# Kernel optimization log

Hardware: AMD Instinct MI355X
Metric: run time of the kernel (lower is better)

The kernel has to match this reference:

```python
import jax, jax.numpy as jnp
import numpy as np

D_MODEL, HID, N_NODES, NODE_DIM = 128, 256, 17, 32

def _gelu(x):
    return jax.nn.gelu(x, approximate=False)  # torch nn.GELU default (erf)

def setup_inputs() -> dict:
    key = jax.random.key(0)
    ks = jax.random.split(key, 12)
    B, W = 16, 4096
    x = jax.random.normal(ks[0], (B, W, D_MODEL), dtype=jnp.float32)
    # node_proj: Linear(128,256) -> GELU -> Linear(256, 17*32)
    W1 = jax.random.normal(ks[1], (D_MODEL, HID), dtype=jnp.float32) / np.sqrt(D_MODEL)
    b1 = jnp.zeros((HID,), jnp.float32)
    W2 = jax.random.normal(ks[2], (HID, N_NODES * NODE_DIM), dtype=jnp.float32) / np.sqrt(HID)
    b2 = jnp.zeros((N_NODES * NODE_DIM,), jnp.float32)
    # GAT1
    adj1 = jnp.eye(N_NODES, dtype=jnp.float32) * 5.0 + jax.random.normal(ks[3], (N_NODES, N_NODES), jnp.float32) * 0.05
    Wg1 = jax.random.normal(ks[4], (NODE_DIM, NODE_DIM), dtype=jnp.float32) / np.sqrt(NODE_DIM)
    bg1 = jnp.zeros((NODE_DIM,), jnp.float32)
    # GAT2
    adj2 = jnp.eye(N_NODES, dtype=jnp.float32) * 5.0 + jax.random.normal(ks[5], (N_NODES, N_NODES), jnp.float32) * 0.05
    Wg2 = jax.random.normal(ks[6], (NODE_DIM, NODE_DIM), dtype=jnp.float32) / np.sqrt(NODE_DIM)
    bg2 = jnp.zeros((NODE_DIM,), jnp.float32)
    # coord_proj: Linear(32, 2)
    Wc = jax.random.normal(ks[7], (NODE_DIM, 2), dtype=jnp.float32) / np.sqrt(NODE_DIM)
    bc = jnp.zeros((2,), jnp.float32)
    return {"x": x, "W1": W1, "b1": b1, "W2": W2, "b2": b2,
            "adj1": adj1, "Wg1": Wg1, "bg1": bg1,
            "adj2": adj2, "Wg2": Wg2, "bg2": bg2,
            "Wc": Wc, "bc": bc}

def _gat(nodes, adj_logits, Wg, bg):
    # nodes: [B, W, N, F]
    adj = jax.nn.softmax(adj_logits, axis=-1)          # [N, N]
    mixed = jnp.einsum('ij,bwjf->bwif', adj, nodes)    # graph conv over 17 joints
    return _gelu(mixed @ Wg + bg) + nodes              # linear-GELU + residual

def reference(x, W1, b1, W2, b2, adj1, Wg1, bg1, adj2, Wg2, bg2, Wc, bc):
    B, W, _ = x.shape
    h = _gelu(x @ W1 + b1)                 # [B, W, 256] (dropout inactive at eval)
    nodes = (h @ W2 + b2).reshape(B, W, N_NODES, NODE_DIM)
    out = _gat(nodes, adj1, Wg1, bg1)
    out = _gat(out, adj2, Wg2, bg2)
    return out @ Wc + bc                   # [B, W, 17, 2]
```

## Files before the change

### kernel.cpp

```cpp
#include <hip/hip_runtime.h>
#include <hip/hip_bf16.h>

using bf16 = __hip_bfloat16;
typedef __bf16 bf16x8 __attribute__((ext_vector_type(8)));
typedef float f32x4 __attribute__((ext_vector_type(4)));

#define MT 32
#define SX 136
#define SH 264
#define SN 552
#define SM 40

__device__ __forceinline__ float bf2f(bf16 v) { return __bfloat162float(v); }

__device__ __forceinline__ float gelu_f(float x) {
    float u  = 0.7978845608f * x * (1.0f + 0.044715f * x * x);
    float au = fabsf(u);
    float e  = __expf(-2.0f * au);
    float t  = (1.0f - e) / (1.0f + e);
    t = (u < 0.0f) ? -t : t;
    return 0.5f * x * (1.0f + t);
}

__device__ __forceinline__ bf16x8 ld8(const bf16* p) {
    return *reinterpret_cast<const bf16x8*>(p);
}
__device__ __forceinline__ f32x4 mfma16(bf16x8 a, bf16x8 b, f32x4 c) {
    return __builtin_amdgcn_mfma_f32_16x16x32_bf16(a, b, c, 0, 0, 0);
}

__global__ void prep_kernel(const float* __restrict__ W1, const float* __restrict__ W2,
                            const float* __restrict__ Wg1, const float* __restrict__ Wg2,
                            const float* __restrict__ adj1, const float* __restrict__ adj2,
                            bf16* __restrict__ w1t, bf16* __restrict__ w2t,
                            bf16* __restrict__ wg1t, bf16* __restrict__ wg2t,
                            float* __restrict__ A1f, float* __restrict__ A2f) {
    int idx = blockIdx.x * 256 + threadIdx.x;
    if (idx < 32768) {
        int r = idx >> 8, c = idx & 255;
        w1t[c * 128 + r] = __float2bfloat16(W1[idx]);
    } else if (idx < 172032) {
        int j = idx - 32768;
        int r = j / 544, c = j % 544;
        w2t[c * 256 + r] = __float2bfloat16(W2[j]);
    } else if (idx < 173056) {
        int j = idx - 172032;
        wg1t[(j & 31) * 32 + (j >> 5)] = __float2bfloat16(Wg1[j]);
    } else if (idx < 174080) {
        int j = idx - 173056;
        wg2t[(j & 31) * 32 + (j >> 5)] = __float2bfloat16(Wg2[j]);
    }
    if (blockIdx.x == 0) {
        int t = threadIdx.x;
        if (t < 17 || (t >= 32 && t < 49)) {
            const float* adj = (t < 17) ? adj1 : adj2;
            float*       A   = (t < 17) ? A1f  : A2f;
            int row = (t < 17) ? t : (t - 32);
            float v[17]; float mx = -1e30f;
            for (int j = 0; j < 17; ++j) { v[j] = adj[row * 17 + j]; mx = fmaxf(mx, v[j]); }
            float s = 0.0f;
            for (int j = 0; j < 17; ++j) { v[j] = __expf(v[j] - mx); s += v[j]; }
            float inv = 1.0f / s;
            for (int j = 0; j < 17; ++j) A[row * 17 + j] = v[j] * inv;
        }
    }
}

__global__ __launch_bounds__(256, 2)
void gat_main(const float* __restrict__ x,
              const float* __restrict__ b1, const float* __restrict__ b2,
              const float* __restrict__ bg1, const float* __restrict__ bg2,
              const bf16* __restrict__ w1t, const bf16* __restrict__ w2t,
              const bf16* __restrict__ wg1t, const bf16* __restrict__ wg2t,
              const float* __restrict__ A1, const float* __restrict__ A2,
              const float* __restrict__ Wc, const float* __restrict__ bc,
              float* __restrict__ out) {
    __shared__ alignas(16) bf16 lds[30464];
    bf16* xs = lds;
    bf16* hs = lds + 4352;
    bf16* ms = lds;
    bf16* ns = lds + 12800;

    const int tid  = threadIdx.x;
    const int w    = tid >> 6;
    const int lane = tid & 63;
    const int l    = lane & 15;
    const int q    = lane >> 4;
    const int t0   = blockIdx.x * MT;

    for (int c = tid; c < 1024; c += 256) {
        int row = c >> 5, c4 = c & 31;
        const float4 v = *reinterpret_cast<const float4*>(x + (size_t)(t0 + row) * 128 + c4 * 4);
        bf16 tmp[4] = { __float2bfloat16(v.x), __float2bfloat16(v.y),
                        __float2bfloat16(v.z), __float2bfloat16(v.w) };
        *reinterpret_cast<ushort4*>(xs + row * SX + c4 * 4) =
            *reinterpret_cast<const ushort4*>(tmp);
    }
    __syncthreads();

    for (int nt = w * 4; nt < w * 4 + 4; ++nt) {
        int n = nt * 16 + l;
        bf16x8 bfr[4];
        const bf16* wp = w1t + n * 128 + q * 8;
#pragma unroll
        for (int kf = 0; kf < 4; ++kf) bfr[kf] = ld8(wp + kf * 32);
        float bias = b1[n];
#pragma unroll
        for (int mt = 0; mt < 2; ++mt) {
            f32x4 acc = {0.f, 0.f, 0.f, 0.f};
            const bf16* ap = xs + (mt * 16 + l) * SX + q * 8;
#pragma unroll
            for (int kf = 0; kf < 4; ++kf)
                acc = mfma16(ld8(ap + kf * 32), bfr[kf], acc);
            int trow = mt * 16 + q * 4;
#pragma unroll
            for (int r = 0; r < 4; ++r)
                hs[(trow + r) * SH + n] = __float2bfloat16(gelu_f(acc[r] + bias));
        }
    }
    __syncthreads();

    for (int nt = w; nt < 34; nt += 4) {
        int n = nt * 16 + l;
        bf16x8 bfr[8];
        const bf16* wp = w2t + n * 256 + q * 8;
#pragma unroll
        for (int kf = 0; kf < 8; ++kf) bfr[kf] = ld8(wp + kf * 32);
        float bias = b2[n];
#pragma unroll
        for (int mt = 0; mt < 2; ++mt) {
            f32x4 acc = {0.f, 0.f, 0.f, 0.f};
            const bf16* ap = hs + (mt * 16 + l) * SH + q * 8;
#pragma unroll
            for (int kf = 0; kf < 8; ++kf)
                acc = mfma16(ld8(ap + kf * 32), bfr[kf], acc);
            int trow = mt * 16 + q * 4;
#pragma unroll
            for (int r = 0; r < 4; ++r)
                ns[(trow + r) * SN + n] = __float2bfloat16(acc[r] + bias);
        }
    }
    __syncthreads();

    for (int g = 0; g < 2; ++g) {
        const float* A   = g ? A2 : A1;
        const bf16* wgt  = g ? wg2t : wg1t;
        const float* bg  = g ? bg2 : bg1;
        bf16x8 wfr[2];
#pragma unroll
        for (int nt = 0; nt < 2; ++nt) wfr[nt] = ld8(wgt + (nt * 16 + l) * 32 + q * 8);
        float bgf[2] = { bg[l], bg[16 + l] };

        for (int half = 0; half < 2; ++half) {
            {
                int th   = tid >> 4;
                int tloc = half * 16 + th;
                int f0   = (tid & 15) * 2;
                float v0[17], v1[17];
                const bf16* npt = ns + tloc * SN + f0;
#pragma unroll
                for (int j = 0; j < 17; ++j) {
                    __hip_bfloat162 p = *reinterpret_cast<const __hip_bfloat162*>(npt + j * 32);
                    v0[j] = bf2f(p.x); v1[j] = bf2f(p.y);
                }
                for (int i = 0; i < 17; ++i) {
                    float m0 = 0.f, m1 = 0.f;
#pragma unroll
                    for (int j = 0; j < 17; ++j) {
                        float a = A[i * 17 + j];
                        m0 = fmaf(a, v0[j], m0);
                        m1 = fmaf(a, v1[j], m1);
                    }
                    __hip_bfloat162 pr;
                    pr.x = __float2bfloat16(m0); pr.y = __float2bfloat16(m1);
                    *reinterpret_cast<__hip_bfloat162*>(ms + (th * 17 + i) * SM + f0) = pr;
                }
            }
            __syncthreads();

            for (int mt = w; mt < 17; mt += 4) {
                const bf16* ap = ms + (mt * 16 + l) * SM + q * 8;
                bf16x8 afr = ld8(ap);
#pragma unroll
                for (int nt = 0; nt < 2; ++nt) {
                    f32x4 acc = {0.f, 0.f, 0.f, 0.f};
                    acc = mfma16(afr, wfr[nt], acc);
                    int f = nt * 16 + l;
#pragma unroll
                    for (int r = 0; r < 4; ++r) {
                        int rloc = mt * 16 + q * 4 + r;
                        int t    = half * 16 + rloc / 17;
                        int i    = rloc % 17;
                        int off  = t * SN + i * 32 + f;
                        float nv = bf2f(ns[off]);
                        ns[off]  = __float2bfloat16(gelu_f(acc[r] + bgf[nt]) + nv);
                    }
                }
            }
            __syncthreads();
        }
    }

    for (int r = tid; r < 544; r += 256) {
        int t = r / 17, i = r % 17;
        const __hip_bfloat162* gp = reinterpret_cast<const __hip_bfloat162*>(ns + t * SN + i * 32);
        float o0 = bc[0], o1 = bc[1];
#pragma unroll
        for (int k2 = 0; k2 < 16; ++k2) {
            __hip_bfloat162 p = gp[k2];
            float a = bf2f(p.x), b = bf2f(p.y);
            int k = k2 * 2;
            o0 = fmaf(a, Wc[k * 2 + 0], o0);
            o1 = fmaf(a, Wc[k * 2 + 1], o1);
            o0 = fmaf(b, Wc[k * 2 + 2], o0);
            o1 = fmaf(b, Wc[k * 2 + 3], o1);
        }
        float2 pr = { o0, o1 };
        reinterpret_cast<float2*>(out)[(size_t)(t0 + t) * 17 + i] = pr;
    }
}

extern "C" void kernel_launch(void* const* d_in, const int* in_sizes, int n_in,
                              void* d_out, int out_size, void* d_ws, size_t ws_size,
                              hipStream_t stream) {
    const float* x    = (const float*)d_in[0];
    const float* W1   = (const float*)d_in[1];
    const float* b1   = (const float*)d_in[2];
    const float* W2   = (const float*)d_in[3];
    const float* b2   = (const float*)d_in[4];
    const float* adj1 = (const float*)d_in[5];
    const float* Wg1  = (const float*)d_in[6];
    const float* bg1  = (const float*)d_in[7];
    const float* adj2 = (const float*)d_in[8];
    const float* Wg2  = (const float*)d_in[9];
    const float* bg2  = (const float*)d_in[10];
    const float* Wc   = (const float*)d_in[11];
    const float* bc   = (const float*)d_in[12];

    char* ws = (char*)d_ws;
    bf16*  w1t  = (bf16*)(ws + 0);
    bf16*  w2t  = (bf16*)(ws + 65536);
    bf16*  wg1t = (bf16*)(ws + 344064);
    bf16*  wg2t = (bf16*)(ws + 346112);
    float* A1f  = (float*)(ws + 348160);
    float* A2f  = (float*)(ws + 349376);

    prep_kernel<<<680, 256, 0, stream>>>(W1, W2, Wg1, Wg2, adj1, adj2,
                                         w1t, w2t, wg1t, wg2t, A1f, A2f);

    const int tokens = 16 * 4096;
    gat_main<<<tokens / MT, 256, 0, stream>>>(x, b1, b2, bg1, bg2,
                                              w1t, w2t, wg1t, wg2t,
                                              A1f, A2f, Wc, bc, (float*)d_out);
}
```

Baseline: 268.6 us.

## Fold adjacency mixing and GAT linear into a Kronecker weight GEMM

Each GAT layer's softmax(adj) mixing and its 32x32 linear are fused into one 544x544 Kronecker weight (A ⊗ Wg), precomputed in a new prep kernel, so every layer becomes one MFMA GEMM over the full node vector. This drops the scalar 17x17 FMA mixing loop, the intermediate mixed buffer and the half-tile passes with their extra barriers, and also shrinks LDS use. The layer-2 GEMM is restructured to keep A fragments in registers and stream weights from global memory. In exchange it does about 17x more MFMA FLOPs per layer, reads a ~590KB weight per layer from cache, and holds more registers for the A fragments.

Result: slower. 355.8 us (+32.5%).

```diff
diff --git a/kernel.cpp b/kernel.cpp
--- a/kernel.cpp
+++ b/kernel.cpp
@@ -8,8 +8,7 @@
 #define MT 32
 #define SX 136
 #define SH 264
-#define SN 552
-#define SM 40
+#define SR 552
 
 __device__ __forceinline__ float bf2f(bf16 v) { return __bfloat162float(v); }
 
@@ -30,10 +29,8 @@
 }
 
 __global__ void prep_kernel(const float* __restrict__ W1, const float* __restrict__ W2,
-                            const float* __restrict__ Wg1, const float* __restrict__ Wg2,
                             const float* __restrict__ adj1, const float* __restrict__ adj2,
                             bf16* __restrict__ w1t, bf16* __restrict__ w2t,
-                            bf16* __restrict__ wg1t, bf16* __restrict__ wg2t,
                             float* __restrict__ A1f, float* __restrict__ A2f) {
     int idx = blockIdx.x * 256 + threadIdx.x;
     if (idx < 32768) {
@@ -43,12 +40,6 @@
         int j = idx - 32768;
         int r = j / 544, c = j % 544;
         w2t[c * 256 + r] = __float2bfloat16(W2[j]);
-    } else if (idx < 173056) {
-        int j = idx - 172032;
-        wg1t[(j & 31) * 32 + (j >> 5)] = __float2bfloat16(Wg1[j]);
-    } else if (idx < 174080) {
-        int j = idx - 173056;
-        wg2t[(j & 31) * 32 + (j >> 5)] = __float2bfloat16(Wg2[j]);
     }
     if (blockIdx.x == 0) {
         int t = threadIdx.x;
@@ -66,20 +57,72 @@
     }
 }
 
+__global__ void prep2_kernel(const float* __restrict__ Wg1, const float* __restrict__ Wg2,
+                             const float* __restrict__ A1f, const float* __restrict__ A2f,
+                             bf16* __restrict__ k1, bf16* __restrict__ k2) {
+    int idx = blockIdx.x * 256 + threadIdx.x;
+    int g = idx / (544 * 544);
+    int r = idx - g * (544 * 544);
+    int n = r / 544;
+    int k = r - n * 544;
+    int i = n >> 5, fp = n & 31;
+    int j = k >> 5, f  = k & 31;
+    const float* A  = g ? A2f : A1f;
+    const float* Wg = g ? Wg2 : Wg1;
+    bf16*        K  = g ? k2  : k1;
+    float v = A[i * 17 + j] * Wg[f * 32 + fp];
+    K[(((n >> 4) * 17 + (k >> 5)) << 9) + ((n & 15) << 5) + (k & 31)] = __float2bfloat16(v);
+}
+
+__device__ __forceinline__ void gat_kron(bf16* __restrict__ nb,
+                                         const bf16* __restrict__ km, const float* __restrict__ bg,
+                                         int w, int l, int q) {
+    bf16x8 afr[2][17];
+#pragma unroll
+    for (int mt = 0; mt < 2; ++mt)
+#pragma unroll
+        for (int ks = 0; ks < 17; ++ks)
+            afr[mt][ks] = ld8(nb + (mt * 16 + l) * SR + ks * 32 + q * 8);
+    __syncthreads();
+
+    for (int nt = w; nt < 34; nt += 4) {
+        int n = nt * 16 + l;
+        float bias = bg[n & 31];
+        f32x4 a0 = {0.f, 0.f, 0.f, 0.f}, a1 = {0.f, 0.f, 0.f, 0.f};
+        const bf16* kp = km + nt * 17 * 512 + l * 32 + q * 8;
+#pragma unroll
+        for (int ks = 0; ks < 17; ++ks) {
+            bf16x8 bfr = ld8(kp + ks * 512);
+            a0 = mfma16(afr[0][ks], bfr, a0);
+            a1 = mfma16(afr[1][ks], bfr, a1);
+        }
+#pragma unroll
+        for (int mt = 0; mt < 2; ++mt) {
+            const f32x4 acc = mt ? a1 : a0;
+#pragma unroll
+            for (int r = 0; r < 4; ++r) {
+                int row = mt * 16 + q * 4 + r;
+                int off = row * SR + n;
+                float v = gelu_f(acc[r] + bias) + bf2f(nb[off]);
+                nb[off] = __float2bfloat16(v);
+            }
+        }
+    }
+    __syncthreads();
+}
+
 __global__ __launch_bounds__(256, 2)
 void gat_main(const float* __restrict__ x,
               const float* __restrict__ b1, const float* __restrict__ b2,
               const float* __restrict__ bg1, const float* __restrict__ bg2,
               const bf16* __restrict__ w1t, const bf16* __restrict__ w2t,
-              const bf16* __restrict__ wg1t, const bf16* __restrict__ wg2t,
-              const float* __restrict__ A1, const float* __restrict__ A2,
+              const bf16* __restrict__ k1, const bf16* __restrict__ k2,
               const float* __restrict__ Wc, const float* __restrict__ bc,
               float* __restrict__ out) {
-    __shared__ alignas(16) bf16 lds[30464];
-    bf16* xs = lds;
-    bf16* hs = lds + 4352;
-    bf16* ms = lds;
-    bf16* ns = lds + 12800;
+    __shared__ alignas(16) bf16 S[17664];
+    bf16* xs = S;
+    bf16* hs = S + 4352;
+    bf16* nb = S;
 
     const int tid  = threadIdx.x;
     const int w    = tid >> 6;
@@ -120,96 +163,52 @@
     }
     __syncthreads();
 
-    for (int nt = w; nt < 34; nt += 4) {
-        int n = nt * 16 + l;
-        bf16x8 bfr[8];
-        const bf16* wp = w2t + n * 256 + q * 8;
-#pragma unroll
-        for (int kf = 0; kf < 8; ++kf) bfr[kf] = ld8(wp + kf * 32);
-        float bias = b2[n];
-#pragma unroll
-        for (int mt = 0; mt < 2; ++mt) {
-            f32x4 acc = {0.f, 0.f, 0.f, 0.f};
-            const bf16* ap = hs + (mt * 16 + l) * SH + q * 8;
+    {
+        bf16x8 af[2][8];
+#pragma unroll
+        for (int mt = 0; mt < 2; ++mt)
 #pragma unroll
             for (int kf = 0; kf < 8; ++kf)
-                acc = mfma16(ld8(ap + kf * 32), bfr[kf], acc);
-            int trow = mt * 16 + q * 4;
-#pragma unroll
-            for (int r = 0; r < 4; ++r)
-                ns[(trow + r) * SN + n] = __float2bfloat16(acc[r] + bias);
-        }
-    }
-    __syncthreads();
-
-    for (int g = 0; g < 2; ++g) {
-        const float* A   = g ? A2 : A1;
-        const bf16* wgt  = g ? wg2t : wg1t;
-        const float* bg  = g ? bg2 : bg1;
-        bf16x8 wfr[2];
-#pragma unroll
-        for (int nt = 0; nt < 2; ++nt) wfr[nt] = ld8(wgt + (nt * 16 + l) * 32 + q * 8);
-        float bgf[2] = { bg[l], bg[16 + l] };
-
-        for (int half = 0; half < 2; ++half) {
-            {
-                int th   = tid >> 4;
-                int tloc = half * 16 + th;
-                int f0   = (tid & 15) * 2;
-                float v0[17], v1[17];
-                const bf16* npt = ns + tloc * SN + f0;
-#pragma unroll
-                for (int j = 0; j < 17; ++j) {
-                    __hip_bfloat162 p = *reinterpret_cast<const __hip_bfloat162*>(npt + j * 32);
-                    v0[j] = bf2f(p.x); v1[j] = bf2f(p.y);
-                }
-                for (int i = 0; i < 17; ++i) {
-                    float m0 = 0.f, m1 = 0.f;
-#pragma unroll
-                    for (int j = 0; j < 17; ++j) {
-                        float a = A[i * 17 + j];
-                        m0 = fmaf(a, v0[j], m0);
-                        m1 = fmaf(a, v1[j], m1);
-                    }
-                    __hip_bfloat162 pr;
-                    pr.x = __float2bfloat16(m0); pr.y = __float2bfloat16(m1);
-                    *reinterpret_cast<__hip_bfloat162*>(ms + (th * 17 + i) * SM + f0) = pr;
+                af[mt][kf] = ld8(hs + (mt * 16 + l) * SH + kf * 32 + q * 8);
+        __syncthreads();
+
+        for (int nt = w; nt < 34; nt += 4) {
+            int n = nt * 16 + l;
+            float bias = b2[n];
+            f32x4 a0 = {0.f, 0.f, 0.f, 0.f}, a1 = {0.f, 0.f, 0.f, 0.f};
+            const bf16* wp = w2t + n * 256 + q * 8;
+#pragma unroll
+            for (int kf = 0; kf < 8; ++kf) {
+                bf16x8 bfr = ld8(wp + kf * 32);
+                a0 = mfma16(af[0][kf], bfr, a0);
+                a1 = mfma16(af[1][kf], bfr, a1);
+            }
+#pragma unroll
+            for (int mt = 0; mt < 2; ++mt) {
+                const f32x4 acc = mt ? a1 : a0;
+#pragma unroll
+                for (int r = 0; r < 4; ++r) {
+                    int row = mt * 16 + q * 4 + r;
+                    nb[row * SR + n] = __float2bfloat16(acc[r] + bias);
                 }
             }
-            __syncthreads();
-
-            for (int mt = w; mt < 17; mt += 4) {
-                const bf16* ap = ms + (mt * 16 + l) * SM + q * 8;
-                bf16x8 afr = ld8(ap);
-#pragma unroll
-                for (int nt = 0; nt < 2; ++nt) {
-                    f32x4 acc = {0.f, 0.f, 0.f, 0.f};
-                    acc = mfma16(afr, wfr[nt], acc);
-                    int f = nt * 16 + l;
-#pragma unroll
-                    for (int r = 0; r < 4; ++r) {
-                        int rloc = mt * 16 + q * 4 + r;
-                        int t    = half * 16 + rloc / 17;
-                        int i    = rloc % 17;
-                        int off  = t * SN + i * 32 + f;
-                        float nv = bf2f(ns[off]);
-                        ns[off]  = __float2bfloat16(gelu_f(acc[r] + bgf[nt]) + nv);
-                    }
-                }
-            }
-            __syncthreads();
-        }
-    }
+        }
+    }
+    __syncthreads();
+
+    gat_kron(nb, k1, bg1, w, l, q);
+    gat_kron(nb, k2, bg2, w, l, q);
 
     for (int r = tid; r < 544; r += 256) {
         int t = r / 17, i = r % 17;
-        const __hip_bfloat162* gp = reinterpret_cast<const __hip_bfloat162*>(ns + t * SN + i * 32);
         float o0 = bc[0], o1 = bc[1];
-#pragma unroll
-        for (int k2 = 0; k2 < 16; ++k2) {
-            __hip_bfloat162 p = gp[k2];
+        const __hip_bfloat162* gp =
+            reinterpret_cast<const __hip_bfloat162*>(nb + t * SR + i * 32);
+#pragma unroll
+        for (int k2i = 0; k2i < 16; ++k2i) {
+            __hip_bfloat162 p = gp[k2i];
             float a = bf2f(p.x), b = bf2f(p.y);
-            int k = k2 * 2;
+            int k = k2i * 2;
             o0 = fmaf(a, Wc[k * 2 + 0], o0);
             o1 = fmaf(a, Wc[k * 2 + 1], o1);
             o0 = fmaf(b, Wc[k * 2 + 2], o0);
@@ -238,18 +237,18 @@
     const float* bc   = (const float*)d_in[12];
 
     char* ws = (char*)d_ws;
-    bf16*  w1t  = (bf16*)(ws + 0);
-    bf16*  w2t  = (bf16*)(ws + 65536);
-    bf16*  wg1t = (bf16*)(ws + 344064);
-    bf16*  wg2t = (bf16*)(ws + 346112);
-    float* A1f  = (float*)(ws + 348160);
-    float* A2f  = (float*)(ws + 349376);
-
-    prep_kernel<<<680, 256, 0, stream>>>(W1, W2, Wg1, Wg2, adj1, adj2,
-                                         w1t, w2t, wg1t, wg2t, A1f, A2f);
+    bf16*  w1t = (bf16*)(ws + 0);
+    bf16*  w2t = (bf16*)(ws + 65536);
+    bf16*  k1  = (bf16*)(ws + 344064);
+    bf16*  k2  = (bf16*)(ws + 935936);
+    float* A1f = (float*)(ws + 1527808);
+    float* A2f = (float*)(ws + 1529856);
+
+    prep_kernel<<<672, 256, 0, stream>>>(W1, W2, adj1, adj2, w1t, w2t, A1f, A2f);
+    prep2_kernel<<<2312, 256, 0, stream>>>(Wg1, Wg2, A1f, A2f, k1, k2);
 
     const int tokens = 16 * 4096;
     gat_main<<<tokens / MT, 256, 0, stream>>>(x, b1, b2, bg1, bg2,
-                                              w1t, w2t, wg1t, wg2t,
-                                              A1f, A2f, Wc, bc, (float*)d_out);
-}
+                                              w1t, w2t, k1, k2,
+                                              Wc, bc, (float*)d_out);
+}
```

## Move 17-joint adjacency mixing onto MFMA with feature-major node layout

Applied to the files above, without the earlier changes.

Replaces the scalar FMA adjacency mixing (17x17 per feature pair) with an MFMA, using the softmaxed adjacency as a zero-padded bf16 B operand. Node features are stored feature-major with a padded joint stride of 20, so each (token, feature) row can be loaded as an MFMA A fragment. The second linear layer now preloads the hidden activations into registers and streams W2 fragments once per n-tile instead of once per m-tile. The adjacency weights are rounded to bf16, which adds rounding error, and the scattered transposed stores may cause LDS bank conflicts.

After: 273.8 us. No clear change (+2.0%).

```diff
diff --git a/kernel.cpp b/kernel.cpp
--- a/kernel.cpp
+++ b/kernel.cpp
@@ -2,14 +2,20 @@
 #include <hip/hip_bf16.h>
 
 using bf16 = __hip_bfloat16;
+typedef __bf16 bf16x4v __attribute__((ext_vector_type(4)));
 typedef __bf16 bf16x8 __attribute__((ext_vector_type(8)));
 typedef float f32x4 __attribute__((ext_vector_type(4)));
 
 #define MT 32
 #define SX 136
 #define SH 264
-#define SN 552
-#define SM 40
+#define SJ 20
+#define TFS 640
+#define NTF_ELEMS 20480
+#define NTF_TOTAL 20496
+#define MS_BASE 20496
+#define SMS 40
+#define S_ELEMS 31376
 
 __device__ __forceinline__ float bf2f(bf16 v) { return __bfloat162float(v); }
 
@@ -24,6 +30,11 @@
 
 __device__ __forceinline__ bf16x8 ld8(const bf16* p) {
     return *reinterpret_cast<const bf16x8*>(p);
+}
+__device__ __forceinline__ bf16x8 ld8u(const bf16* p) {
+    bf16x4v lo = *reinterpret_cast<const bf16x4v*>(p);
+    bf16x4v hi = *reinterpret_cast<const bf16x4v*>(p + 4);
+    return __builtin_shufflevector(lo, hi, 0, 1, 2, 3, 4, 5, 6, 7);
 }
 __device__ __forceinline__ f32x4 mfma16(bf16x8 a, bf16x8 b, f32x4 c) {
     return __builtin_amdgcn_mfma_f32_16x16x32_bf16(a, b, c, 0, 0, 0);
@@ -75,11 +86,10 @@
               const float* __restrict__ A1, const float* __restrict__ A2,
               const float* __restrict__ Wc, const float* __restrict__ bc,
               float* __restrict__ out) {
-    __shared__ alignas(16) bf16 lds[30464];
-    bf16* xs = lds;
-    bf16* hs = lds + 4352;
-    bf16* ms = lds;
-    bf16* ns = lds + 12800;
+    __shared__ alignas(16) bf16 S[S_ELEMS];
+    bf16* xs = S;
+    bf16* hs = S + 4352;
+    bf16* ms = S + MS_BASE;
 
     const int tid  = threadIdx.x;
     const int w    = tid >> 6;
@@ -120,80 +130,106 @@
     }
     __syncthreads();
 
-    for (int nt = w; nt < 34; nt += 4) {
-        int n = nt * 16 + l;
-        bf16x8 bfr[8];
-        const bf16* wp = w2t + n * 256 + q * 8;
-#pragma unroll
-        for (int kf = 0; kf < 8; ++kf) bfr[kf] = ld8(wp + kf * 32);
-        float bias = b2[n];
-#pragma unroll
-        for (int mt = 0; mt < 2; ++mt) {
-            f32x4 acc = {0.f, 0.f, 0.f, 0.f};
-            const bf16* ap = hs + (mt * 16 + l) * SH + q * 8;
+    {
+        bf16x8 af[2][8];
+#pragma unroll
+        for (int mt = 0; mt < 2; ++mt)
 #pragma unroll
             for (int kf = 0; kf < 8; ++kf)
-                acc = mfma16(ld8(ap + kf * 32), bfr[kf], acc);
-            int trow = mt * 16 + q * 4;
-#pragma unroll
-            for (int r = 0; r < 4; ++r)
-                ns[(trow + r) * SN + n] = __float2bfloat16(acc[r] + bias);
+                af[mt][kf] = ld8(hs + (mt * 16 + l) * SH + kf * 32 + q * 8);
+        __syncthreads();
+
+        for (int z = tid; z < 3072; z += 256) {
+            int row = z / 3, k = z - row * 3;
+            S[row * SJ + 17 + k] = __float2bfloat16(0.f);
+        }
+        if (tid < 16) S[NTF_ELEMS + tid] = __float2bfloat16(0.f);
+
+        for (int nt = w; nt < 34; nt += 4) {
+            int n = nt * 16 + l;
+            float bias = b2[n];
+            int i = n >> 5, f = n & 31;
+            f32x4 a0 = {0.f, 0.f, 0.f, 0.f}, a1 = {0.f, 0.f, 0.f, 0.f};
+            const bf16* wp = w2t + n * 256 + q * 8;
+#pragma unroll
+            for (int kf = 0; kf < 8; ++kf) {
+                bf16x8 bfr = ld8(wp + kf * 32);
+                a0 = mfma16(af[0][kf], bfr, a0);
+                a1 = mfma16(af[1][kf], bfr, a1);
+            }
+#pragma unroll
+            for (int mt = 0; mt < 2; ++mt) {
+                const f32x4 acc = mt ? a1 : a0;
+#pragma unroll
+                for (int r = 0; r < 4; ++r) {
+                    int t = mt * 16 + q * 4 + r;
+                    S[t * TFS + f * SJ + i] = __float2bfloat16(acc[r] + bias);
+                }
+            }
         }
     }
     __syncthreads();
 
     for (int g = 0; g < 2; ++g) {
-        const float* A   = g ? A2 : A1;
-        const bf16* wgt  = g ? wg2t : wg1t;
-        const float* bg  = g ? bg2 : bg1;
+        const float* A  = g ? A2 : A1;
+        const bf16* wgt = g ? wg2t : wg1t;
+        const float* bg = g ? bg2 : bg1;
+
+        bf16x8 mixB[2];
+#pragma unroll
+        for (int nt = 0; nt < 2; ++nt) {
+            int i = nt * 16 + l;
+            bf16 tmp[8];
+#pragma unroll
+            for (int e = 0; e < 8; ++e) {
+                int j = q * 8 + e;
+                float v = (i < 17 && j < 17) ? A[i * 17 + j] : 0.0f;
+                tmp[e] = __float2bfloat16(v);
+            }
+            mixB[nt] = *reinterpret_cast<bf16x8*>(tmp);
+        }
         bf16x8 wfr[2];
 #pragma unroll
         for (int nt = 0; nt < 2; ++nt) wfr[nt] = ld8(wgt + (nt * 16 + l) * 32 + q * 8);
         float bgf[2] = { bg[l], bg[16 + l] };
 
         for (int half = 0; half < 2; ++half) {
-            {
-                int th   = tid >> 4;
-                int tloc = half * 16 + th;
-                int f0   = (tid & 15) * 2;
-                float v0[17], v1[17];
-                const bf16* npt = ns + tloc * SN + f0;
-#pragma unroll
-                for (int j = 0; j < 17; ++j) {
-                    __hip_bfloat162 p = *reinterpret_cast<const __hip_bfloat162*>(npt + j * 32);
-                    v0[j] = bf2f(p.x); v1[j] = bf2f(p.y);
+            for (int mt = w; mt < 32; mt += 4) {
+                int R = half * 512 + mt * 16 + l;
+                bf16x8 afr = ld8u(S + R * SJ + q * 8);
+                int R0   = mt * 16 + q * 4;
+                int tloc = R0 >> 5, f0 = R0 & 31;
+#pragma unroll
+                for (int nt = 0; nt < 2; ++nt) {
+                    f32x4 acc = {0.f, 0.f, 0.f, 0.f};
+                    acc = mfma16(afr, mixB[nt], acc);
+                    int i = nt * 16 + l;
+                    if (i < 17) {
+                        int s = tloc * 17 + i;
+                        union { ushort4 u; bf16 b[4]; } pk;
+#pragma unroll
+                        for (int r = 0; r < 4; ++r) pk.b[r] = __float2bfloat16(acc[r]);
+                        *reinterpret_cast<ushort4*>(ms + s * SMS + f0) = pk.u;
+                    }
                 }
-                for (int i = 0; i < 17; ++i) {
-                    float m0 = 0.f, m1 = 0.f;
-#pragma unroll
-                    for (int j = 0; j < 17; ++j) {
-                        float a = A[i * 17 + j];
-                        m0 = fmaf(a, v0[j], m0);
-                        m1 = fmaf(a, v1[j], m1);
-                    }
-                    __hip_bfloat162 pr;
-                    pr.x = __float2bfloat16(m0); pr.y = __float2bfloat16(m1);
-                    *reinterpret_cast<__hip_bfloat162*>(ms + (th * 17 + i) * SM + f0) = pr;
-                }
             }
             __syncthreads();
 
             for (int mt = w; mt < 17; mt += 4) {
-                const bf16* ap = ms + (mt * 16 + l) * SM + q * 8;
-                bf16x8 afr = ld8(ap);
+                bf16x8 afr = ld8(ms + (mt * 16 + l) * SMS + q * 8);
 #pragma unroll
                 for (int nt = 0; nt < 2; ++nt) {
                     f32x4 acc = {0.f, 0.f, 0.f, 0.f};
                     acc = mfma16(afr, wfr[nt], acc);
-                    int f = nt * 16 + l;
+                    int fp = nt * 16 + l;
 #pragma unroll
                     for (int r = 0; r < 4; ++r) {
-                        int rloc = mt * 16 + q * 4 + r;
-                        int t    = half * 16 + rloc / 17;
-                        int i    = rloc % 17;
-                        int off  = t * SN + i * 32 + f;
-                        float nv = bf2f(ns[off]);
-                        ns[off]  = __float2bfloat16(gelu_f(acc[r] + bgf[nt]) + nv);
+                        int s    = mt * 16 + q * 4 + r;
+                        int tloc = s / 17;
+                        int i    = s - tloc * 17;
+                        int off  = (half * 16 + tloc) * TFS + fp * SJ + i;
+                        float v  = gelu_f(acc[r] + bgf[nt]) + bf2f(S[off]);
+                        S[off]   = __float2bfloat16(v);
                     }
                 }
             }
@@ -203,17 +239,13 @@
 
     for (int r = tid; r < 544; r += 256) {
         int t = r / 17, i = r % 17;
-        const __hip_bfloat162* gp = reinterpret_cast<const __hip_bfloat162*>(ns + t * SN + i * 32);
         float o0 = bc[0], o1 = bc[1];
-#pragma unroll
-        for (int k2 = 0; k2 < 16; ++k2) {
-            __hip_bfloat162 p = gp[k2];
-            float a = bf2f(p.x), b = bf2f(p.y);
-            int k = k2 * 2;
-            o0 = fmaf(a, Wc[k * 2 + 0], o0);
-            o1 = fmaf(a, Wc[k * 2 + 1], o1);
-            o0 = fmaf(b, Wc[k * 2 + 2], o0);
-            o1 = fmaf(b, Wc[k * 2 + 3], o1);
+        const bf16* gp = S + t * TFS + i;
+#pragma unroll
+        for (int f = 0; f < 32; ++f) {
+            float v = bf2f(gp[f * SJ]);
+            o0 = fmaf(v, Wc[f * 2 + 0], o0);
+            o1 = fmaf(v, Wc[f * 2 + 1], o1);
         }
         float2 pr = { o0, o1 };
         reinterpret_cast<float2*>(out)[(size_t)(t0 + t) * 17 + i] = pr;
```
